# Optimization experiments

Hardware: AMD Instinct MI355X
Metric: run time of the kernel (lower is better)

The kernel has to match this reference:

```python
import jax, jax.numpy as jnp
import numpy as np

IOU_THRESHOLD = 0.5  # default in ObjectUtils.nms
N_BOXES = 10000


def setup_inputs() -> dict:
    key = jax.random.key(0)
    k1, k2 = jax.random.split(key)
    boxes = jax.random.uniform(k1, (N_BOXES, 4), dtype=jnp.float32)  # normalized cxcywh
    scores = jax.random.uniform(k2, (N_BOXES,), dtype=jnp.float32)
    return {"boxes_cxcywh": boxes, "scores": scores}


def _cxcywh_to_ltrb(b):
    cx, cy, w, h = b[:, 0], b[:, 1], b[:, 2], b[:, 3]
    return jnp.stack([cx - w / 2, cy - h / 2, cx + w / 2, cy + h / 2], axis=1)


def _pairwise_iou(a, b):
    # a: [N1,4] ltrb, b: [N2,4] ltrb -> [N1,N2] (matches ObjectUtils.compute_iou)
    lt = jnp.maximum(a[:, None, :2], b[None, :, :2])
    rb = jnp.minimum(a[:, None, 2:], b[None, :, 2:])
    wh = jnp.clip(rb - lt, 0.0)
    inter = wh[..., 0] * wh[..., 1]
    area_a = (a[:, 2] - a[:, 0]) * (a[:, 3] - a[:, 1])
    area_b = (b[:, 2] - b[:, 0]) * (b[:, 3] - b[:, 1])
    return inter / (area_a[:, None] + area_b[None, :] - inter)


def reference(boxes_cxcywh, scores):
    ltrb = _cxcywh_to_ltrb(boxes_cxcywh)
    iou = _pairwise_iou(ltrb, ltrb)  # [N,N]

    # ---- greedy NMS, faithful to ObjectUtils.nms (unclamped intersection,
    # retain when iou < threshold) expressed as a jit-friendly suppression loop ----
    n = ltrb.shape[0]
    order = jnp.argsort(-scores)  # highest score first (torch.sort ascending, pop last)
    bs = ltrb[order]
    l, t, r, b = bs[:, 0], bs[:, 1], bs[:, 2], bs[:, 3]
    area = (r - l) * (b - t)
    inter_nms = (jnp.minimum(r[:, None], r[None, :]) - jnp.maximum(l[:, None], l[None, :])) * \
                (jnp.minimum(b[:, None], b[None, :]) - jnp.maximum(t[:, None], t[None, :]))
    iou_nms = inter_nms / (area[:, None] + area[None, :] - inter_nms)
    ar = jnp.arange(n)

    def body(i, keep):
        # box i (in sorted order) suppresses lower-scored boxes only if it is itself kept
        suppress = keep[i] & (iou_nms[i] >= IOU_THRESHOLD) & (ar > i)
        return keep & jnp.logical_not(suppress)

    keep_sorted = jax.lax.fori_loop(0, n, body, jnp.ones((n,), dtype=bool))
    keep = jnp.zeros((n,), dtype=bool).at[order].set(keep_sorted)
    return iou, keep
```

## Files before the change

### kernel.cpp

```cpp
#include <hip/hip_runtime.h>

typedef unsigned long long u64;

#define THR 0.5f

__device__ __forceinline__ void conv_box(const float4 b, float& l, float& t,
                                         float& r, float& bo, float& a) {
  #pragma clang fp contract(off)
  float hw = 0.5f * b.z;
  float hh = 0.5f * b.w;
  l = b.x - hw;
  t = b.y - hh;
  r = b.x + hw;
  bo = b.y + hh;
  a = (r - l) * (bo - t);
}

__global__ void k_zero(int* __restrict__ rank, int n) {
  int i = blockIdx.x * blockDim.x + threadIdx.x;
  if (i < n) rank[i] = 0;
}

__global__ void k_rank(const float* __restrict__ scores, int* __restrict__ rank,
                       int n, int jchunk) {
  int i = blockIdx.x * blockDim.x + threadIdx.x;
  if (i >= n) return;
  float si = scores[i];
  int j0 = blockIdx.y * jchunk;
  int j1 = min(j0 + jchunk, n);
  int c = 0;
  for (int j = j0; j < j1; ++j) {
    float sj = scores[j];
    c += ((sj > si) || (sj == si && j < i)) ? 1 : 0;
  }
  if (c) atomicAdd(rank + i, c);
}

__global__ void k_scatter(const float4* __restrict__ boxes, const int* __restrict__ rank,
                          float* __restrict__ sl, float* __restrict__ st,
                          float* __restrict__ sr, float* __restrict__ sb,
                          float* __restrict__ sa, int* __restrict__ sidx, int n) {
  int i = blockIdx.x * blockDim.x + threadIdx.x;
  if (i >= n) return;
  float l, t, r, b, a;
  conv_box(boxes[i], l, t, r, b, a);
  int k = rank[i];
  sl[k] = l; st[k] = t; sr[k] = r; sb[k] = b; sa[k] = a; sidx[k] = i;
}

__global__ void k_mask(const float* __restrict__ sl, const float* __restrict__ st,
                       const float* __restrict__ sr, const float* __restrict__ sb,
                       const float* __restrict__ sa,
                       u64* __restrict__ mask, u64* __restrict__ diag,
                       u64* __restrict__ band, int n, int wstride) {
  #pragma clang fp contract(off)
  int k = blockIdx.x * blockDim.x + threadIdx.x;
  if (k >= n) return;
  int w = blockIdx.y;
  int jbase = w << 6;
  u64 word = 0;
  if (jbase + 63 > k) {
    float l = sl[k], t = st[k], r = sr[k], b = sb[k], a = sa[k];
    int jend = min(jbase + 64, n);
    for (int j = max(jbase, k + 1); j < jend; ++j) {
      float lmax = fmaxf(l, sl[j]);
      float tmax = fmaxf(t, st[j]);
      float rmin = fminf(r, sr[j]);
      float bmin = fminf(b, sb[j]);
      float wd = rmin - lmax;
      float hd = bmin - tmax;
      float inter = wd * hd;
      float denom = (a + sa[j]) - inter;
      float q = inter / denom;
      if (q >= THR) word |= 1ull << (j - jbase);
    }
  }
  mask[(size_t)k * wstride + w] = word;
  int kg = k >> 6;
  if (kg == w) diag[k] = word;
  if (w == kg + 1) band[k] = word;
}

__device__ __forceinline__ u64 wave_or_u64(u64 v) {
  unsigned lo = (unsigned)v, hi = (unsigned)(v >> 32);
#define DPP_OR(x, ctrl, rmask) \
  x |= (unsigned)__builtin_amdgcn_update_dpp(0, (int)(x), ctrl, rmask, 0xF, true)
  DPP_OR(lo, 0x111, 0xF); DPP_OR(hi, 0x111, 0xF);
  DPP_OR(lo, 0x112, 0xF); DPP_OR(hi, 0x112, 0xF);
  DPP_OR(lo, 0x114, 0xF); DPP_OR(hi, 0x114, 0xF);
  DPP_OR(lo, 0x118, 0xF); DPP_OR(hi, 0x118, 0xF);
  DPP_OR(lo, 0x142, 0xA); DPP_OR(hi, 0x142, 0xA);
  DPP_OR(lo, 0x143, 0xC); DPP_OR(hi, 0x143, 0xC);
#undef DPP_OR
  unsigned flo = (unsigned)__builtin_amdgcn_readlane((int)lo, 63);
  unsigned fhi = (unsigned)__builtin_amdgcn_readlane((int)hi, 63);
  return ((u64)fhi << 32) | flo;
}

__device__ __forceinline__ void scan_body7(
    const u64* __restrict__ mask, const u64* __restrict__ diag,
    const u64* __restrict__ band, const int* __restrict__ sidx,
    float* __restrict__ keep, int n, int wstride,
    u64* rem, u64* dsh, u64* bsh, u64* kwords, int (*kept)[64], int* nk_sh) {
  int t = threadIdx.x, wv = t >> 6, lane = t & 63;
  int ng = (n + 63) >> 6;
  rem[t] = 0;
  if (t < 2) nk_sh[t] = 0;
  u64 bnd = 0;
  u64 x0 = 0, x1 = 0, x2 = 0, x3 = 0, x4 = 0, x5 = 0, x6 = 0, x7 = 0;
  const ulonglong2* d2 = (const ulonglong2*)dsh;
  if (wv == 0) {
    dsh[lane] = diag[lane];
    bsh[lane] = band[lane];
    ulonglong2 p0 = d2[0], p1 = d2[1], p2 = d2[2], p3 = d2[3];
    x0 = p0.x; x1 = p0.y; x2 = p1.x; x3 = p1.y;
    x4 = p2.x; x5 = p2.y; x6 = p3.x; x7 = p3.y;
  }
  __syncthreads();
  for (int g = 0; g < ng; ++g) {
    int base = g << 6;
    if (wv == 0) {
      int nxt = base + 64 + lane;
      u64 dnext = (g + 1 < ng) ? diag[nxt] : 0;
      u64 bnext = (g + 1 < ng) ? band[nxt] : 0;
      u64 bshv = bsh[lane];
      u64 s = rem[g] | bnd;
      int valid = n - base;
      if (valid < 64) s |= (~0ull) << valid;
      u64 kw = 0;
      u64 y0, y1, y2, y3, y4, y5, y6, y7;
#define LDC(a0,a1,a2,a3,a4,a5,a6,a7, c) { \
      ulonglong2 q0 = d2[4*(c)], q1 = d2[4*(c)+1], q2 = d2[4*(c)+2], q3 = d2[4*(c)+3]; \
      a0 = q0.x; a1 = q0.y; a2 = q1.x; a3 = q1.y; a4 = q2.x; a5 = q2.y; a6 = q3.x; a7 = q3.y; }
#define STEP(BB, EQ) if (!((s >> (BB)) & 1ull)) { kw |= 1ull << (BB); s |= EQ; }
#define CHUNK(b0v, a0,a1,a2,a3,a4,a5,a6,a7) \
      if ((unsigned)((s >> (b0v)) & 0xFFull) != 0xFFu) { \
        STEP(b0v+0, a0) STEP(b0v+1, a1) STEP(b0v+2, a2) STEP(b0v+3, a3) \
        STEP(b0v+4, a4) STEP(b0v+5, a5) STEP(b0v+6, a6) STEP(b0v+7, a7) }
      LDC(y0,y1,y2,y3,y4,y5,y6,y7, 1); CHUNK(0,  x0,x1,x2,x3,x4,x5,x6,x7);
      LDC(x0,x1,x2,x3,x4,x5,x6,x7, 2); CHUNK(8,  y0,y1,y2,y3,y4,y5,y6,y7);
      LDC(y0,y1,y2,y3,y4,y5,y6,y7, 3); CHUNK(16, x0,x1,x2,x3,x4,x5,x6,x7);
      LDC(x0,x1,x2,x3,x4,x5,x6,x7, 4); CHUNK(24, y0,y1,y2,y3,y4,y5,y6,y7);
      LDC(y0,y1,y2,y3,y4,y5,y6,y7, 5); CHUNK(32, x0,x1,x2,x3,x4,x5,x6,x7);
      LDC(x0,x1,x2,x3,x4,x5,x6,x7, 6); CHUNK(40, y0,y1,y2,y3,y4,y5,y6,y7);
      LDC(y0,y1,y2,y3,y4,y5,y6,y7, 7); CHUNK(48, x0,x1,x2,x3,x4,x5,x6,x7);
                                       CHUNK(56, y0,y1,y2,y3,y4,y5,y6,y7);
#undef CHUNK
#undef STEP
#undef LDC
      if (lane == 0) kwords[g] = kw;
      int nk = __popcll(kw);
      if ((kw >> lane) & 1ull) {
        int pos = __popcll(kw & ((1ull << lane) - 1ull));
        kept[g & 1][pos] = lane;
      }
      int npad = (nk + 15) & ~15;
      if (lane >= nk && lane < npad) kept[g & 1][lane] = 0;
      if (lane == 0) nk_sh[g & 1] = nk;
      u64 bv = ((kw >> lane) & 1ull) ? bshv : 0ull;
      bnd = wave_or_u64(bv);
      dsh[lane] = dnext;
      bsh[lane] = bnext;
      ulonglong2 p0 = d2[0], p1 = d2[1], p2 = d2[2], p3 = d2[3];
      x0 = p0.x; x1 = p0.y; x2 = p1.x; x3 = p1.y;
      x4 = p2.x; x5 = p2.y; x6 = p3.x; x7 = p3.y;
    } else {
      int w = t - 64;
      int gp = g - 1;
      if (gp >= 0 && w > g && w < ng) {
        int nkp = nk_sh[gp & 1];
        if (nkp) {
          const int* kp = kept[gp & 1];
          int basep = gp << 6;
          u64 acc = 0;
          for (int i = 0; i < nkp; i += 16) {
            int k0 = kp[i+0],  k1 = kp[i+1],  k2 = kp[i+2],  k3 = kp[i+3];
            int k4 = kp[i+4],  k5 = kp[i+5],  k6 = kp[i+6],  k7 = kp[i+7];
            int k8 = kp[i+8],  k9 = kp[i+9],  k10 = kp[i+10], k11 = kp[i+11];
            int k12 = kp[i+12], k13 = kp[i+13], k14 = kp[i+14], k15 = kp[i+15];
            u64 v0 = mask[(size_t)(basep + k0) * wstride + w];
            u64 v1 = mask[(size_t)(basep + k1) * wstride + w];
            u64 v2 = mask[(size_t)(basep + k2) * wstride + w];
            u64 v3 = mask[(size_t)(basep + k3) * wstride + w];
            u64 v4 = mask[(size_t)(basep + k4) * wstride + w];
            u64 v5 = mask[(size_t)(basep + k5) * wstride + w];
            u64 v6 = mask[(size_t)(basep + k6) * wstride + w];
            u64 v7 = mask[(size_t)(basep + k7) * wstride + w];
            u64 v8 = mask[(size_t)(basep + k8) * wstride + w];
            u64 v9 = mask[(size_t)(basep + k9) * wstride + w];
            u64 v10 = mask[(size_t)(basep + k10) * wstride + w];
            u64 v11 = mask[(size_t)(basep + k11) * wstride + w];
            u64 v12 = mask[(size_t)(basep + k12) * wstride + w];
            u64 v13 = mask[(size_t)(basep + k13) * wstride + w];
            u64 v14 = mask[(size_t)(basep + k14) * wstride + w];
            u64 v15 = mask[(size_t)(basep + k15) * wstride + w];
            acc |= v0;
            if (i + 1 < nkp)  acc |= v1;
            if (i + 2 < nkp)  acc |= v2;
            if (i + 3 < nkp)  acc |= v3;
            if (i + 4 < nkp)  acc |= v4;
            if (i + 5 < nkp)  acc |= v5;
            if (i + 6 < nkp)  acc |= v6;
            if (i + 7 < nkp)  acc |= v7;
            if (i + 8 < nkp)  acc |= v8;
            if (i + 9 < nkp)  acc |= v9;
            if (i + 10 < nkp) acc |= v10;
            if (i + 11 < nkp) acc |= v11;
            if (i + 12 < nkp) acc |= v12;
            if (i + 13 < nkp) acc |= v13;
            if (i + 14 < nkp) acc |= v14;
            if (i + 15 < nkp) acc |= v15;
          }
          rem[w] |= acc;
        }
      }
    }
    __syncthreads();
  }
  for (int k = t; k < n; k += 256) {
    u64 kwv = kwords[k >> 6];
    keep[sidx[k]] = ((kwv >> (k & 63)) & 1ull) ? 1.0f : 0.0f;
  }
}

__global__ __launch_bounds__(256, 1) void k_scan2(const u64* __restrict__ mask,
                                                  const u64* __restrict__ diag,
                                                  const u64* __restrict__ band,
                                                  const int* __restrict__ sidx,
                                                  float* __restrict__ keep,
                                                  int n, int wstride) {
  __shared__ u64 rem[256];
  __shared__ __align__(16) u64 dsh[64];
  __shared__ u64 bsh[64];
  __shared__ u64 kwords[160];
  __shared__ int kept[2][64];
  __shared__ int nk_sh[2];
  scan_body7(mask, diag, band, sidx, keep, n, wstride, rem, dsh, bsh, kwords, kept, nk_sh);
}

__device__ __forceinline__ float iou_one(float li, float ti, float ri, float bi, float ai,
                                         float lj, float tj, float rj, float bj, float aj) {
  float lmax = fmaxf(li, lj);
  float tmax = fmaxf(ti, tj);
  float rmin = fminf(ri, rj);
  float bmin = fminf(bi, bj);
  float w = fmaxf(rmin - lmax, 0.0f);
  float h = fmaxf(bmin - tmax, 0.0f);
  float inter = w * h;
  float denom = (ai + aj) - inter;
  return inter * __builtin_amdgcn_rcpf(denom);
}

__device__ __forceinline__ void iou_body(const float4* __restrict__ boxes,
                                         float* __restrict__ out,
                                         int n, int rpb, int bx, int by) {
  int nj4 = (n + 3) >> 2;
  int j4 = bx * 256 + threadIdx.x;
  if (j4 >= nj4) return;
  int j = j4 << 2;
  int jc1 = min(j + 1, n - 1), jc2 = min(j + 2, n - 1), jc3 = min(j + 3, n - 1);
  float l0,t0,r0,b0,a0, l1,t1,r1,b1,a1, l2,t2,r2,b2,a2, l3,t3,r3,b3,a3;
  conv_box(boxes[j],   l0,t0,r0,b0,a0);
  conv_box(boxes[jc1], l1,t1,r1,b1,a1);
  conv_box(boxes[jc2], l2,t2,r2,b2,a2);
  conv_box(boxes[jc3], l3,t3,r3,b3,a3);
  bool full = (j + 3) < n;
  for (int rr = 0; rr < rpb; ++rr) {
    int i = by * rpb + rr;
    if (i >= n) return;
    float li,ti,ri,bi,ai;
    conv_box(boxes[i], li,ti,ri,bi,ai);
    float4 o;
    o.x = iou_one(li,ti,ri,bi,ai, l0,t0,r0,b0,a0);
    o.y = iou_one(li,ti,ri,bi,ai, l1,t1,r1,b1,a1);
    o.z = iou_one(li,ti,ri,bi,ai, l2,t2,r2,b2,a2);
    o.w = iou_one(li,ti,ri,bi,ai, l3,t3,r3,b3,a3);
    size_t row = (size_t)i * n;
    if (full) {
      *reinterpret_cast<float4*>(out + row + j) = o;
    } else {
      out[row + j] = o.x;
      if (j + 1 < n) out[row + j + 1] = o.y;
      if (j + 2 < n) out[row + j + 2] = o.z;
    }
  }
}

__global__ void k_iou(const float4* __restrict__ boxes, float* __restrict__ out,
                      int n, int rpb) {
  iou_body(boxes, out, n, rpb, blockIdx.x, blockIdx.y);
}

__global__ __launch_bounds__(256, 4) void k_fused(const float4* __restrict__ boxes,
                                                  float* __restrict__ out,
                                                  const u64* __restrict__ mask,
                                                  const u64* __restrict__ diag,
                                                  const u64* __restrict__ band,
                                                  const int* __restrict__ sidx,
                                                  float* __restrict__ keep,
                                                  int n, int wstride, int rpb, int gx) {
  __shared__ u64 rem[256];
  __shared__ __align__(16) u64 dsh[64];
  __shared__ u64 bsh[64];
  __shared__ u64 kwords[160];
  __shared__ int kept[2][64];
  __shared__ int nk_sh[2];
  if (blockIdx.x == 0) {
    scan_body7(mask, diag, band, sidx, keep, n, wstride, rem, dsh, bsh, kwords, kept, nk_sh);
    return;
  }
  int id = blockIdx.x - 1;
  iou_body(boxes, out, n, rpb, id % gx, id / gx);
}

extern "C" void kernel_launch(void* const* d_in, const int* in_sizes, int n_in,
                              void* d_out, int out_size, void* d_ws, size_t ws_size,
                              hipStream_t stream) {
  const float* boxes = (const float*)d_in[0];
  const float* scores = (const float*)d_in[1];
  int n = in_sizes[1];
  float* out = (float*)d_out;
  size_t NN = (size_t)n * (size_t)n;
  float* keep = out + NN;

  int words = (n + 63) >> 6;
  int wstride = (words + 3) & ~3;
  size_t need = (size_t)n * wstride * 8
              + (size_t)words * 64 * 8 * 2
              + 256
              + (size_t)n * 4 * 7;
  bool use_ws = (ws_size >= need);

  char* base = use_ws ? (char*)d_ws : (char*)d_out;
  size_t off = 0;
  u64* mask = (u64*)(base + off); off += (size_t)n * wstride * 8;
  u64* diag = (u64*)(base + off); off += (size_t)words * 64 * 8;
  u64* band = (u64*)(base + off); off += (size_t)words * 64 * 8;
  off = (off + 255) & ~(size_t)255;
  float* sl  = (float*)(base + off); off += (size_t)n * 4;
  float* st_ = (float*)(base + off); off += (size_t)n * 4;
  float* sr  = (float*)(base + off); off += (size_t)n * 4;
  float* sb  = (float*)(base + off); off += (size_t)n * 4;
  float* sa  = (float*)(base + off); off += (size_t)n * 4;
  int* sidx  = (int*)(base + off); off += (size_t)n * 4;
  int* rank  = (int*)(base + off); off += (size_t)n * 4;

  int nb = (n + 255) / 256;
  k_zero<<<nb, 256, 0, stream>>>(rank, n);

  int jblocks = 40;
  int jchunk = (n + jblocks - 1) / jblocks;
  k_rank<<<dim3(nb, jblocks), 256, 0, stream>>>(scores, rank, n, jchunk);

  k_scatter<<<nb, 256, 0, stream>>>((const float4*)boxes, rank, sl, st_, sr, sb, sa, sidx, n);

  k_mask<<<dim3(nb, words), 256, 0, stream>>>(sl, st_, sr, sb, sa, mask, diag, band, n, wstride);

  int rpb = 10;
  int nj4 = (n + 3) >> 2;
  int gx = (nj4 + 255) / 256;
  int gy = (n + rpb - 1) / rpb;

  if (use_ws) {
    k_fused<<<gx * gy + 1, 256, 0, stream>>>((const float4*)boxes, out, mask, diag,
                                             band, sidx, keep, n, wstride, rpb, gx);
  } else {
    k_scan2<<<1, 256, 0, stream>>>(mask, diag, band, sidx, keep, n, wstride);
    k_iou<<<dim3(gx, gy), 256, 0, stream>>>((const float4*)boxes, out, n, rpb);
  }
}
```

Before: 389.9 us.

## Fuse mask computation with IoU matrix kernel and run scan afterward

Merges the suppression-mask kernel and the IoU matrix kernel into a single launch with a flat block index split between the two jobs. The greedy scan now runs as a separate single-block kernel after that launch, instead of sharing a launch with the IoU blocks. This hides mask computation behind the bandwidth-bound IoU writes, but exposes the serial scan, which previously overlapped with the IoU work.

```diff
diff --git a/kernel.cpp b/kernel.cpp
--- a/kernel.cpp
+++ b/kernel.cpp
@@ -48,15 +48,16 @@
   sl[k] = l; st[k] = t; sr[k] = r; sb[k] = b; sa[k] = a; sidx[k] = i;
 }
 
-__global__ void k_mask(const float* __restrict__ sl, const float* __restrict__ st,
-                       const float* __restrict__ sr, const float* __restrict__ sb,
-                       const float* __restrict__ sa,
-                       u64* __restrict__ mask, u64* __restrict__ diag,
-                       u64* __restrict__ band, int n, int wstride) {
+__device__ __forceinline__ void mask_body(
+    const float* __restrict__ sl, const float* __restrict__ st,
+    const float* __restrict__ sr, const float* __restrict__ sb,
+    const float* __restrict__ sa,
+    u64* __restrict__ mask, u64* __restrict__ diag, u64* __restrict__ band,
+    int n, int wstride, int bx, int by) {
   #pragma clang fp contract(off)
-  int k = blockIdx.x * blockDim.x + threadIdx.x;
+  int k = bx * 256 + threadIdx.x;
   if (k >= n) return;
-  int w = blockIdx.y;
+  int w = by;
   int jbase = w << 6;
   u64 word = 0;
   if (jbase + 63 > k) {
@@ -79,6 +80,14 @@
   int kg = k >> 6;
   if (kg == w) diag[k] = word;
   if (w == kg + 1) band[k] = word;
+}
+
+__global__ void k_mask(const float* __restrict__ sl, const float* __restrict__ st,
+                       const float* __restrict__ sr, const float* __restrict__ sb,
+                       const float* __restrict__ sa,
+                       u64* __restrict__ mask, u64* __restrict__ diag,
+                       u64* __restrict__ band, int n, int wstride) {
+  mask_body(sl, st, sr, sb, sa, mask, diag, band, n, wstride, blockIdx.x, blockIdx.y);
 }
 
 __device__ __forceinline__ u64 wave_or_u64(u64 v) {
@@ -291,26 +300,21 @@
   iou_body(boxes, out, n, rpb, blockIdx.x, blockIdx.y);
 }
 
-__global__ __launch_bounds__(256, 4) void k_fused(const float4* __restrict__ boxes,
-                                                  float* __restrict__ out,
-                                                  const u64* __restrict__ mask,
-                                                  const u64* __restrict__ diag,
-                                                  const u64* __restrict__ band,
-                                                  const int* __restrict__ sidx,
-                                                  float* __restrict__ keep,
-                                                  int n, int wstride, int rpb, int gx) {
-  __shared__ u64 rem[256];
-  __shared__ __align__(16) u64 dsh[64];
-  __shared__ u64 bsh[64];
-  __shared__ u64 kwords[160];
-  __shared__ int kept[2][64];
-  __shared__ int nk_sh[2];
-  if (blockIdx.x == 0) {
-    scan_body7(mask, diag, band, sidx, keep, n, wstride, rem, dsh, bsh, kwords, kept, nk_sh);
-    return;
-  }
-  int id = blockIdx.x - 1;
-  iou_body(boxes, out, n, rpb, id % gx, id / gx);
+__global__ __launch_bounds__(256) void k_maskiou(
+    const float* __restrict__ sl, const float* __restrict__ st,
+    const float* __restrict__ sr, const float* __restrict__ sb,
+    const float* __restrict__ sa,
+    u64* __restrict__ mask, u64* __restrict__ diag, u64* __restrict__ band,
+    int wstride, const float4* __restrict__ boxes, float* __restrict__ out,
+    int n, int rpb, int nbx, int nmask, int gx) {
+  int id = blockIdx.x;
+  if (id < nmask) {
+    mask_body(sl, st, sr, sb, sa, mask, diag, band, n, wstride,
+              id % nbx, id / nbx);
+  } else {
+    int iid = id - nmask;
+    iou_body(boxes, out, n, rpb, iid % gx, iid / gx);
+  }
 }
 
 extern "C" void kernel_launch(void* const* d_in, const int* in_sizes, int n_in,
@@ -354,17 +358,20 @@
 
   k_scatter<<<nb, 256, 0, stream>>>((const float4*)boxes, rank, sl, st_, sr, sb, sa, sidx, n);
 
-  k_mask<<<dim3(nb, words), 256, 0, stream>>>(sl, st_, sr, sb, sa, mask, diag, band, n, wstride);
-
   int rpb = 10;
   int nj4 = (n + 3) >> 2;
   int gx = (nj4 + 255) / 256;
   int gy = (n + rpb - 1) / rpb;
 
   if (use_ws) {
-    k_fused<<<gx * gy + 1, 256, 0, stream>>>((const float4*)boxes, out, mask, diag,
-                                             band, sidx, keep, n, wstride, rpb, gx);
+    int nmask = nb * words;
+    int total = nmask + gx * gy;
+    k_maskiou<<<total, 256, 0, stream>>>(sl, st_, sr, sb, sa, mask, diag, band,
+                                         wstride, (const float4*)boxes, out,
+                                         n, rpb, nb, nmask, gx);
+    k_scan2<<<1, 256, 0, stream>>>(mask, diag, band, sidx, keep, n, wstride);
   } else {
+    k_mask<<<dim3(nb, words), 256, 0, stream>>>(sl, st_, sr, sb, sa, mask, diag, band, n, wstride);
     k_scan2<<<1, 256, 0, stream>>>(mask, diag, band, sidx, keep, n, wstride);
     k_iou<<<dim3(gx, gy), 256, 0, stream>>>((const float4*)boxes, out, n, rpb);
   }
```

Result: slower. 409.0 us (+4.9%).
